# Kernel tuning notes

Hardware: AMD Instinct MI355X
Metric: run time of the kernel (lower is better)

The kernel has to match this reference:

```python
import jax, jax.numpy as jnp
import numpy as np

NUM_HEADS = 8
HIDDEN = 128
MAX_NEIGHBORS = 64
BATCH = 8192


def setup_inputs() -> dict:
    key = jax.random.key(0)
    ks = jax.random.split(key, 4)
    query = jax.random.normal(ks[0], (BATCH, MAX_NEIGHBORS, HIDDEN), dtype=jnp.float32)
    value = jax.random.normal(ks[1], (BATCH, 1, HIDDEN), dtype=jnp.float32)
    # per-head Dense(hidden) weights (glorot-ish scale) + zero biases
    Wa = jax.random.normal(ks[2], (NUM_HEADS, HIDDEN, HIDDEN), dtype=jnp.float32) * (1.0 / np.sqrt(HIDDEN))
    ba = jnp.zeros((NUM_HEADS, HIDDEN), dtype=jnp.float32)
    Wo = jax.random.normal(ks[3], (NUM_HEADS * HIDDEN, HIDDEN), dtype=jnp.float32) * (1.0 / np.sqrt(NUM_HEADS * HIDDEN))
    bo = jnp.zeros((HIDDEN,), dtype=jnp.float32)
    return {"query": query, "value": value, "Wa": Wa, "ba": ba, "Wo": Wo, "bo": bo}


def reference(query, value, Wa, ba, Wo, bo):
    # query: [B, N, H], value: [B, 1, H]
    q = jnp.concatenate([query, value], axis=1)  # [B, N+1, H]
    contexts = []
    for i in range(NUM_HEADS):
        # sequential per-head projection of the running query tensor
        q = jnp.einsum('bnh,hk->bnk', q, Wa[i]) + ba[i]          # [B, N+1, H]
        e = jnp.einsum('boh,bnh->bon', value, q)                 # [B, 1, N+1]
        scores = jax.nn.softmax(e, axis=-1)                      # [B, 1, N+1]
        contexts.append(jnp.einsum('bon,bnh->boh', scores, q))   # [B, 1, H]
    ctx = jnp.concatenate(contexts, axis=-1)                     # [B, 1, num_heads*H]
    x = jnp.einsum('boc,ck->bok', ctx, Wo) + bo                  # [B, 1, H]
    return jax.nn.relu(x)
```

## Files before the change

kernel.cpp:

```cpp
#include <hip/hip_runtime.h>
#include <math.h>

#define WS_P  0
#define WS_Q0 65536
#define WS_Q1 81920
#define WS_R  98304
#define WS_WT 114688
#define WS_WU 245760
#define WS_ZT 376832
#define WS_Z0 507904
#define WS_U  524288
#define WS_PO 8912896

struct MMJob { const float* A; const float* B; float* C; float* wu; };
struct MMArgs { MMJob j[8]; };

__device__ __forceinline__ float dpp_xor1(float x) {
  return __int_as_float(__builtin_amdgcn_update_dpp(0, __float_as_int(x), 0xB1, 0xF, 0xF, false));
}
__device__ __forceinline__ float dpp_xor2(float x) {
  return __int_as_float(__builtin_amdgcn_update_dpp(0, __float_as_int(x), 0x4E, 0xF, 0xF, false));
}
__device__ __forceinline__ float dpp_xor8(float x) {
  return __int_as_float(__builtin_amdgcn_update_dpp(0, __float_as_int(x), 0x128, 0xF, 0xF, false));
}
__device__ __forceinline__ float readlane_f(float v, int n) {
  return __int_as_float(__builtin_amdgcn_readlane(__float_as_int(v), n));
}

__device__ void mm128_job(const MMJob J, const int tile, const int t, float* Al) {
  const int col = t & 127;
  const int rg = t >> 7;
  if (J.A == nullptr) {
    for (int rr = 0; rr < 16; ++rr) {
      const int r = tile * 32 + rg * 16 + rr;
      const float v = J.B[r * 128 + col];
      if (J.C) J.C[r * 128 + col] = v;
      if (J.wu) J.wu[col * 1024 + r] = v;
    }
    return;
  }
  for (int jj = 0; jj < 16; ++jj) {
    const int idx = t + jj * 256;
    Al[idx] = J.A[tile * 32 * 128 + idx];
  }
  __syncthreads();
  float acc[16];
#pragma unroll
  for (int rr = 0; rr < 16; ++rr) acc[rr] = 0.f;
  for (int h = 0; h < 128; ++h) {
    const float bv = J.B[h * 128 + col];
#pragma unroll
    for (int rr = 0; rr < 16; ++rr)
      acc[rr] = fmaf(Al[(rg * 16 + rr) * 128 + h], bv, acc[rr]);
  }
#pragma unroll
  for (int rr = 0; rr < 16; ++rr) {
    const int r = tile * 32 + rg * 16 + rr;
    if (J.C) J.C[r * 128 + col] = acc[rr];
    if (J.wu) J.wu[col * 1024 + r] = acc[rr];
  }
}

__global__ __launch_bounds__(256) void k1_setup(MMArgs args,
    const float* __restrict__ Wa, const float* __restrict__ ba,
    const float* __restrict__ Wo, const float* __restrict__ bo,
    float* __restrict__ z0) {
  __shared__ float smem[4096];
  const int t = threadIdx.x;
  if (blockIdx.x < 16) {
    mm128_job(args.j[blockIdx.x >> 2], blockIdx.x & 3, t, smem);
    return;
  }
  float* bt = smem;
  float* zpart = smem + 1024;
  if (t < 128) bt[t] = ba[t];
  __syncthreads();
  for (int i = 1; i < 8; ++i) {
    if (t < 128) {
      float v = ba[i * 128 + t];
      for (int h = 0; h < 128; ++h)
        v = fmaf(bt[(i - 1) * 128 + h], Wa[i * 16384 + h * 128 + t], v);
      bt[i * 128 + t] = v;
    }
    __syncthreads();
  }
  const int col = t & 127, half = t >> 7;
  float z = half ? 0.f : bo[col];
  for (int i = half * 4; i < half * 4 + 4; ++i)
    for (int h = 0; h < 128; ++h)
      z = fmaf(bt[i * 128 + h], Wo[(i * 128 + h) * 128 + col], z);
  zpart[half * 128 + col] = z;
  __syncthreads();
  if (t < 128) z0[t] = zpart[t] + zpart[128 + t];
}

__global__ __launch_bounds__(256) void mm128_jobs(MMArgs args) {
  __shared__ float smem[4096];
  mm128_job(args.j[blockIdx.x >> 2], blockIdx.x & 3, threadIdx.x, smem);
}

__device__ void gemm_U_dev(const float* __restrict__ V, const float* __restrict__ WU,
                           float* __restrict__ U, const int bid, const int t, float* Vl) {
  const int rt = bid >> 3;
  const int ct = bid & 7;
  const int cg = t & 7;
  const int rg = t >> 3;
  const int r0 = rt * 128;
  float4 acc[4][4];
#pragma unroll
  for (int a = 0; a < 4; ++a)
#pragma unroll
    for (int c = 0; c < 4; ++c) acc[a][c] = make_float4(0.f, 0.f, 0.f, 0.f);
  for (int kc = 0; kc < 4; ++kc) {
    __syncthreads();
    {
      const int srow = t >> 3, k8 = t & 7;
#pragma unroll
      for (int pp = 0; pp < 4; ++pp) {
        const int rr = pp * 32 + srow;
        *(float4*)&Vl[rr * 33 + k8 * 4] =
            *(const float4*)&V[(size_t)(r0 + rr) * 128 + kc * 32 + k8 * 4];
      }
    }
    __syncthreads();
#pragma unroll 4
    for (int kk = 0; kk < 32; ++kk) {
      const float* wrow = WU + (size_t)(kc * 32 + kk) * 1024 + ct * 128 + cg * 16;
      const float4 w0 = *(const float4*)(wrow + 0);
      const float4 w1 = *(const float4*)(wrow + 4);
      const float4 w2 = *(const float4*)(wrow + 8);
      const float4 w3 = *(const float4*)(wrow + 12);
#pragma unroll
      for (int r = 0; r < 4; ++r) {
        const float s = Vl[(rg * 4 + r) * 33 + kk];
        acc[r][0].x = fmaf(s, w0.x, acc[r][0].x); acc[r][0].y = fmaf(s, w0.y, acc[r][0].y);
        acc[r][0].z = fmaf(s, w0.z, acc[r][0].z); acc[r][0].w = fmaf(s, w0.w, acc[r][0].w);
        acc[r][1].x = fmaf(s, w1.x, acc[r][1].x); acc[r][1].y = fmaf(s, w1.y, acc[r][1].y);
        acc[r][1].z = fmaf(s, w1.z, acc[r][1].z); acc[r][1].w = fmaf(s, w1.w, acc[r][1].w);
        acc[r][2].x = fmaf(s, w2.x, acc[r][2].x); acc[r][2].y = fmaf(s, w2.y, acc[r][2].y);
        acc[r][2].z = fmaf(s, w2.z, acc[r][2].z); acc[r][2].w = fmaf(s, w2.w, acc[r][2].w);
        acc[r][3].x = fmaf(s, w3.x, acc[r][3].x); acc[r][3].y = fmaf(s, w3.y, acc[r][3].y);
        acc[r][3].z = fmaf(s, w3.z, acc[r][3].z); acc[r][3].w = fmaf(s, w3.w, acc[r][3].w);
      }
    }
  }
#pragma unroll
  for (int r = 0; r < 4; ++r) {
    float* urow = U + (size_t)(r0 + rg * 4 + r) * 1024 + ct * 128 + cg * 16;
    *(float4*)(urow + 0) = acc[r][0];
    *(float4*)(urow + 4) = acc[r][1];
    *(float4*)(urow + 8) = acc[r][2];
    *(float4*)(urow + 12) = acc[r][3];
  }
}

__global__ __launch_bounds__(256) void k4_combo(MMArgs args,
    const float* __restrict__ V, const float* __restrict__ WU, float* __restrict__ U) {
  __shared__ float smem[4224];
  const int bid = blockIdx.x;
  if (bid < 32) mm128_job(args.j[bid >> 2], bid & 3, threadIdx.x, smem);
  else gemm_U_dev(V, WU, U, bid - 32, threadIdx.x, smem);
}

#define ATTN_NB 4

__global__ __launch_bounds__(256, 4) void attn_main_k(
    const float* __restrict__ query, const float* __restrict__ value,
    float* __restrict__ U) {
  __shared__ float smem[4948];
  float* sct = smem + 4420;
  const int t = threadIdx.x;
  const int w = t >> 6;
  const int l = t & 63;

  const int sel1 = l & 1, sel2 = (l >> 1) & 1, sel8 = (l >> 3) & 1;
  const int g = ((l >> 2) & 1) | (((l >> 4) & 1) << 1) | (((l >> 5) & 1) << 2);
  const int myhead = 4 * sel1 + 2 * sel2 + sel8;
  const int ebase = myhead * 8 + g;

#pragma unroll 1
  for (int j = 0; j < ATTN_NB; ++j) {
    const int b = blockIdx.x * ATTN_NB + j;

    float2 u2[8];
    {
      const float* ub = U + (size_t)b * 1024 + 2 * l;
#pragma unroll
      for (int i = 0; i < 8; ++i) u2[i] = *(const float2*)(ub + i * 128);
    }
    float2 q2[16];
    {
      const float* qb = query + (size_t)b * 8192 + (size_t)(w * 16) * 128 + 2 * l;
#pragma unroll
      for (int r = 0; r < 16; ++r) q2[r] = *(const float2*)(qb + r * 128);
    }
    const float2 v2 = *(const float2*)(value + (size_t)b * 128 + 2 * l);

    auto epass = [&](const float2 qv, const int n) {
      float p[8];
#pragma unroll
      for (int i = 0; i < 8; ++i) p[i] = fmaf(qv.y, u2[i].y, qv.x * u2[i].x);
      float a4[4];
#pragma unroll
      for (int i = 0; i < 4; ++i) {
        const float yours = sel1 ? p[i] : p[i + 4];
        const float mine = sel1 ? p[i + 4] : p[i];
        a4[i] = mine + dpp_xor1(yours);
      }
      float a2v[2];
#pragma unroll
      for (int i = 0; i < 2; ++i) {
        const float yours = sel2 ? a4[i] : a4[i + 2];
        const float mine = sel2 ? a4[i + 2] : a4[i];
        a2v[i] = mine + dpp_xor2(yours);
      }
      const float yours = sel8 ? a2v[0] : a2v[1];
      const float mine = sel8 ? a2v[1] : a2v[0];
      smem[n * 68 + ebase] = mine + dpp_xor8(yours);
    };
#pragma unroll
    for (int r = 0; r < 16; ++r) epass(q2[r], 16 * w + r);
    if (w == 0) epass(v2, 64);
    __syncthreads();

#pragma unroll
    for (int ii = 0; ii < 2; ++ii) {
      const int i = 2 * w + ii;
      const float4 e0 = *(const float4*)&smem[l * 68 + i * 8];
      const float4 e1 = *(const float4*)&smem[l * 68 + i * 8 + 4];
      const float4 f0 = *(const float4*)&smem[64 * 68 + i * 8];
      const float4 f1 = *(const float4*)&smem[64 * 68 + i * 8 + 4];
      const float x = ((e0.x + e0.y) + (e0.z + e0.w)) + ((e1.x + e1.y) + (e1.z + e1.w));
      const float x64 = ((f0.x + f0.y) + (f0.z + f0.w)) + ((f1.x + f1.y) + (f1.z + f1.w));
      float m = x;
      m = fmaxf(m, dpp_xor1(m));
      m = fmaxf(m, dpp_xor2(m));
      m = fmaxf(m, __shfl_xor(m, 4));
      m = fmaxf(m, dpp_xor8(m));
      m = fmaxf(m, __shfl_xor(m, 16));
      m = fmaxf(m, __shfl_xor(m, 32));
      m = fmaxf(m, x64);
      const float p = __expf(x - m);
      const float p64 = __expf(x64 - m);
      float ss = p;
      ss += dpp_xor1(ss);
      ss += dpp_xor2(ss);
      ss += __shfl_xor(ss, 4);
      ss += dpp_xor8(ss);
      ss += __shfl_xor(ss, 16);
      ss += __shfl_xor(ss, 32);
      ss += p64;
      const float inv = 1.0f / ss;
      sct[i * 66 + l] = p * inv;
      if (l == 0) sct[i * 66 + 64] = p64 * inv;
    }
    __syncthreads();

    float sc[8], c64[8];
#pragma unroll
    for (int i = 0; i < 8; ++i) sc[i] = sct[i * 66 + l];
#pragma unroll
    for (int i = 0; i < 8; ++i) c64[i] = sct[i * 66 + 64];

    float2 s2[8];
#pragma unroll
    for (int i = 0; i < 8; ++i) s2[i] = make_float2(0.f, 0.f);
#pragma unroll
    for (int r = 0; r < 16; ++r) {
      const int n = 16 * w + r;
#pragma unroll
      for (int i = 0; i < 8; ++i) {
        const float cwv = readlane_f(sc[i], n);
        s2[i].x = fmaf(cwv, q2[r].x, s2[i].x);
        s2[i].y = fmaf(cwv, q2[r].y, s2[i].y);
      }
    }
    if (w == 0) {
#pragma unroll
      for (int i = 0; i < 8; ++i) {
        s2[i].x = fmaf(c64[i], v2.x, s2[i].x);
        s2[i].y = fmaf(c64[i], v2.y, s2[i].y);
      }
    }
#pragma unroll
    for (int i = 0; i < 8; ++i)
      *(float2*)&smem[w * 1024 + i * 128 + 2 * l] = s2[i];
    __syncthreads();
    float4 acc = make_float4(0.f, 0.f, 0.f, 0.f);
#pragma unroll
    for (int w4 = 0; w4 < 4; ++w4) {
      const float4 pp = *(const float4*)&smem[w4 * 1024 + t * 4];
      acc.x += pp.x; acc.y += pp.y; acc.z += pp.z; acc.w += pp.w;
    }
    *(float4*)(U + (size_t)b * 1024 + t * 4) = acc;
    __syncthreads();
  }
}

__global__ __launch_bounds__(256) void gemm_out_k(
    const float* __restrict__ S, const float* __restrict__ Z,
    float* __restrict__ P0, float* __restrict__ PW) {
  __shared__ float STl[64 * 68];
  const int rb = blockIdx.x >> 2;
  const int kc = blockIdx.x & 3;
  const int t = threadIdx.x;
  const int rg = t >> 4;
  const int cg = t & 15;
  float4 acc[4][2];
#pragma unroll
  for (int r = 0; r < 4; ++r) {
    acc[r][0] = make_float4(0.f, 0.f, 0.f, 0.f);
    acc[r][1] = make_float4(0.f, 0.f, 0.f, 0.f);
  }
  for (int sub = 0; sub < 4; ++sub) {
    const int kb = kc * 256 + sub * 64;
    __syncthreads();
#pragma unroll
    for (int j = 0; j < 4; ++j) {
      const int i4 = t + j * 256;
      const int row = i4 >> 4, kq = i4 & 15;
      const float4 s4 = *(const float4*)&S[(size_t)(rb * 64 + row) * 1024 + kb + kq * 4];
      STl[(kq * 4 + 0) * 68 + row] = s4.x;
      STl[(kq * 4 + 1) * 68 + row] = s4.y;
      STl[(kq * 4 + 2) * 68 + row] = s4.z;
      STl[(kq * 4 + 3) * 68 + row] = s4.w;
    }
    __syncthreads();
#pragma unroll 4
    for (int k = 0; k < 64; ++k) {
      const float4 sa = *(const float4*)&STl[k * 68 + rg * 4];
      const float* zr = Z + (size_t)(kb + k) * 128 + cg * 8;
      const float4 za = *(const float4*)zr;
      const float4 zb = *(const float4*)(zr + 4);
      const float sr[4] = {sa.x, sa.y, sa.z, sa.w};
#pragma unroll
      for (int r = 0; r < 4; ++r) {
        acc[r][0].x = fmaf(sr[r], za.x, acc[r][0].x);
        acc[r][0].y = fmaf(sr[r], za.y, acc[r][0].y);
        acc[r][0].z = fmaf(sr[r], za.z, acc[r][0].z);
        acc[r][0].w = fmaf(sr[r], za.w, acc[r][0].w);
        acc[r][1].x = fmaf(sr[r], zb.x, acc[r][1].x);
        acc[r][1].y = fmaf(sr[r], zb.y, acc[r][1].y);
        acc[r][1].z = fmaf(sr[r], zb.z, acc[r][1].z);
        acc[r][1].w = fmaf(sr[r], zb.w, acc[r][1].w);
      }
    }
  }
  float* P = (kc == 0) ? P0 : (PW + (size_t)(kc - 1) * 1048576);
#pragma unroll
  for (int r = 0; r < 4; ++r) {
    float* prow = P + (size_t)(rb * 64 + rg * 4 + r) * 128 + cg * 8;
    *(float4*)(prow + 0) = acc[r][0];
    *(float4*)(prow + 4) = acc[r][1];
  }
}

__global__ __launch_bounds__(256) void reduce_relu_k(
    float* __restrict__ out, const float* __restrict__ PW,
    const float* __restrict__ z0) {
  const int idx = blockIdx.x * 256 + threadIdx.x;
  const float4 z4 = *(const float4*)&z0[(idx & 31) * 4];
  float4 a = ((const float4*)out)[idx];
  const float4 p1 = ((const float4*)(PW + 0 * 1048576))[idx];
  const float4 p2 = ((const float4*)(PW + 1 * 1048576))[idx];
  const float4 p3 = ((const float4*)(PW + 2 * 1048576))[idx];
  a.x = fmaxf(a.x + p1.x + p2.x + p3.x + z4.x, 0.f);
  a.y = fmaxf(a.y + p1.y + p2.y + p3.y + z4.y, 0.f);
  a.z = fmaxf(a.z + p1.z + p2.z + p3.z + z4.z, 0.f);
  a.w = fmaxf(a.w + p1.w + p2.w + p3.w + z4.w, 0.f);
  ((float4*)out)[idx] = a;
}

extern "C" void kernel_launch(void* const* d_in, const int* in_sizes, int n_in,
                              void* d_out, int out_size, void* d_ws, size_t ws_size,
                              hipStream_t stream) {
  const float* query = (const float*)d_in[0];
  const float* value = (const float*)d_in[1];
  const float* Wa    = (const float*)d_in[2];
  const float* ba    = (const float*)d_in[3];
  const float* Wo    = (const float*)d_in[4];
  const float* bo    = (const float*)d_in[5];
  float* ws = (float*)d_ws;
  float* P  = ws + WS_P;
  float* Q0 = ws + WS_Q0;
  float* Q1 = ws + WS_Q1;
  float* R  = ws + WS_R;
  float* WT = ws + WS_WT;
  float* WU = ws + WS_WU;
  float* ZT = ws + WS_ZT;
  float* Z0 = ws + WS_Z0;
  float* U  = ws + WS_U;
  float* PW = ws + WS_PO;

  MMArgs a1{};
  for (int j = 0; j < 4; ++j)
    a1.j[j] = MMJob{Wa + 2 * j * 16384, Wa + (2 * j + 1) * 16384, P + j * 16384, nullptr};
  k1_setup<<<17, 256, 0, stream>>>(a1, Wa, ba, Wo, bo, Z0);

  MMArgs a2{};
  a2.j[0] = MMJob{P, P + 16384, Q0, nullptr};
  a2.j[1] = MMJob{P + 2 * 16384, P + 3 * 16384, Q1, nullptr};
  a2.j[2] = MMJob{P + 2 * 16384, Wa + 6 * 16384, R, nullptr};
  mm128_jobs<<<12, 256, 0, stream>>>(a2);

  MMArgs a3{};
  a3.j[0] = MMJob{nullptr, Wa,             WT + 0 * 16384, WU + 0 * 128};
  a3.j[1] = MMJob{nullptr, P,              WT + 1 * 16384, WU + 1 * 128};
  a3.j[2] = MMJob{P,       Wa + 2 * 16384, WT + 2 * 16384, WU + 2 * 128};
  a3.j[3] = MMJob{nullptr, Q0,             WT + 3 * 16384, WU + 3 * 128};
  a3.j[4] = MMJob{Q0,      Wa + 4 * 16384, WT + 4 * 16384, WU + 4 * 128};
  a3.j[5] = MMJob{Q0,      P + 2 * 16384,  WT + 5 * 16384, WU + 5 * 128};
  a3.j[6] = MMJob{Q0,      R,              WT + 6 * 16384, WU + 6 * 128};
  a3.j[7] = MMJob{Q0,      Q1,             WT + 7 * 16384, WU + 7 * 128};
  mm128_jobs<<<32, 256, 0, stream>>>(a3);

  MMArgs a4{};
  for (int i = 0; i < 8; ++i)
    a4.j[i] = MMJob{WT + i * 16384, Wo + i * 16384, ZT + i * 16384, nullptr};
  k4_combo<<<544, 256, 0, stream>>>(a4, value, WU, U);

  attn_main_k<<<8192 / ATTN_NB, 256, 0, stream>>>(query, value, U);

  gemm_out_k<<<512, 256, 0, stream>>>(U, ZT, (float*)d_out, PW);
  reduce_relu_k<<<1024, 256, 0, stream>>>((float*)d_out, PW, Z0);
}
```

Before: 265.0 us.

## Launch one attention block per batch row and move bias chain into combo kernel

```diff
diff --git a/kernel.cpp b/kernel.cpp
--- a/kernel.cpp
+++ b/kernel.cpp
@@ -62,16 +62,14 @@
   }
 }
 
-__global__ __launch_bounds__(256) void k1_setup(MMArgs args,
-    const float* __restrict__ Wa, const float* __restrict__ ba,
-    const float* __restrict__ Wo, const float* __restrict__ bo,
-    float* __restrict__ z0) {
+__global__ __launch_bounds__(256) void mm128_jobs(MMArgs args) {
   __shared__ float smem[4096];
-  const int t = threadIdx.x;
-  if (blockIdx.x < 16) {
-    mm128_job(args.j[blockIdx.x >> 2], blockIdx.x & 3, t, smem);
-    return;
-  }
+  mm128_job(args.j[blockIdx.x >> 2], blockIdx.x & 3, threadIdx.x, smem);
+}
+
+__device__ void bias_z0_dev(const float* __restrict__ Wa, const float* __restrict__ ba,
+                            const float* __restrict__ Wo, const float* __restrict__ bo,
+                            float* __restrict__ z0, const int t, float* smem) {
   float* bt = smem;
   float* zpart = smem + 1024;
   if (t < 128) bt[t] = ba[t];
@@ -93,11 +91,6 @@
   zpart[half * 128 + col] = z;
   __syncthreads();
   if (t < 128) z0[t] = zpart[t] + zpart[128 + t];
-}
-
-__global__ __launch_bounds__(256) void mm128_jobs(MMArgs args) {
-  __shared__ float smem[4096];
-  mm128_job(args.j[blockIdx.x >> 2], blockIdx.x & 3, threadIdx.x, smem);
 }
 
 __device__ void gemm_U_dev(const float* __restrict__ V, const float* __restrict__ WU,
@@ -156,20 +149,23 @@
 }
 
 __global__ __launch_bounds__(256) void k4_combo(MMArgs args,
-    const float* __restrict__ V, const float* __restrict__ WU, float* __restrict__ U) {
+    const float* __restrict__ V, const float* __restrict__ WU, float* __restrict__ U,
+    const float* __restrict__ Wa, const float* __restrict__ ba,
+    const float* __restrict__ Wo, const float* __restrict__ bo,
+    float* __restrict__ z0) {
   __shared__ float smem[4224];
   const int bid = blockIdx.x;
   if (bid < 32) mm128_job(args.j[bid >> 2], bid & 3, threadIdx.x, smem);
-  else gemm_U_dev(V, WU, U, bid - 32, threadIdx.x, smem);
-}
-
-#define ATTN_NB 4
+  else if (bid < 544) gemm_U_dev(V, WU, U, bid - 32, threadIdx.x, smem);
+  else bias_z0_dev(Wa, ba, Wo, bo, z0, threadIdx.x, smem);
+}
 
 __global__ __launch_bounds__(256, 4) void attn_main_k(
     const float* __restrict__ query, const float* __restrict__ value,
     float* __restrict__ U) {
   __shared__ float smem[4948];
   float* sct = smem + 4420;
+  const int b = blockIdx.x;
   const int t = threadIdx.x;
   const int w = t >> 6;
   const int l = t & 63;
@@ -179,123 +175,107 @@
   const int myhead = 4 * sel1 + 2 * sel2 + sel8;
   const int ebase = myhead * 8 + g;
 
-#pragma unroll 1
-  for (int j = 0; j < ATTN_NB; ++j) {
-    const int b = blockIdx.x * ATTN_NB + j;
-
-    float2 u2[8];
-    {
-      const float* ub = U + (size_t)b * 1024 + 2 * l;
-#pragma unroll
-      for (int i = 0; i < 8; ++i) u2[i] = *(const float2*)(ub + i * 128);
-    }
-    float2 q2[16];
-    {
-      const float* qb = query + (size_t)b * 8192 + (size_t)(w * 16) * 128 + 2 * l;
-#pragma unroll
-      for (int r = 0; r < 16; ++r) q2[r] = *(const float2*)(qb + r * 128);
-    }
-    const float2 v2 = *(const float2*)(value + (size_t)b * 128 + 2 * l);
-
-    auto epass = [&](const float2 qv, const int n) {
-      float p[8];
-#pragma unroll
-      for (int i = 0; i < 8; ++i) p[i] = fmaf(qv.y, u2[i].y, qv.x * u2[i].x);
-      float a4[4];
-#pragma unroll
-      for (int i = 0; i < 4; ++i) {
-        const float yours = sel1 ? p[i] : p[i + 4];
-        const float mine = sel1 ? p[i + 4] : p[i];
-        a4[i] = mine + dpp_xor1(yours);
-      }
-      float a2v[2];
-#pragma unroll
-      for (int i = 0; i < 2; ++i) {
-        const float yours = sel2 ? a4[i] : a4[i + 2];
-        const float mine = sel2 ? a4[i + 2] : a4[i];
-        a2v[i] = mine + dpp_xor2(yours);
-      }
-      const float yours = sel8 ? a2v[0] : a2v[1];
-      const float mine = sel8 ? a2v[1] : a2v[0];
-      smem[n * 68 + ebase] = mine + dpp_xor8(yours);
-    };
-#pragma unroll
-    for (int r = 0; r < 16; ++r) epass(q2[r], 16 * w + r);
-    if (w == 0) epass(v2, 64);
-    __syncthreads();
-
-#pragma unroll
-    for (int ii = 0; ii < 2; ++ii) {
-      const int i = 2 * w + ii;
-      const float4 e0 = *(const float4*)&smem[l * 68 + i * 8];
-      const float4 e1 = *(const float4*)&smem[l * 68 + i * 8 + 4];
-      const float4 f0 = *(const float4*)&smem[64 * 68 + i * 8];
-      const float4 f1 = *(const float4*)&smem[64 * 68 + i * 8 + 4];
-      const float x = ((e0.x + e0.y) + (e0.z + e0.w)) + ((e1.x + e1.y) + (e1.z + e1.w));
-      const float x64 = ((f0.x + f0.y) + (f0.z + f0.w)) + ((f1.x + f1.y) + (f1.z + f1.w));
-      float m = x;
-      m = fmaxf(m, dpp_xor1(m));
-      m = fmaxf(m, dpp_xor2(m));
-      m = fmaxf(m, __shfl_xor(m, 4));
-      m = fmaxf(m, dpp_xor8(m));
-      m = fmaxf(m, __shfl_xor(m, 16));
-      m = fmaxf(m, __shfl_xor(m, 32));
-      m = fmaxf(m, x64);
-      const float p = __expf(x - m);
-      const float p64 = __expf(x64 - m);
-      float ss = p;
-      ss += dpp_xor1(ss);
-      ss += dpp_xor2(ss);
-      ss += __shfl_xor(ss, 4);
-      ss += dpp_xor8(ss);
-      ss += __shfl_xor(ss, 16);
-      ss += __shfl_xor(ss, 32);
-      ss += p64;
-      const float inv = 1.0f / ss;
-      sct[i * 66 + l] = p * inv;
-      if (l == 0) sct[i * 66 + 64] = p64 * inv;
-    }
-    __syncthreads();
-
-    float sc[8], c64[8];
-#pragma unroll
-    for (int i = 0; i < 8; ++i) sc[i] = sct[i * 66 + l];
-#pragma unroll
-    for (int i = 0; i < 8; ++i) c64[i] = sct[i * 66 + 64];
-
-    float2 s2[8];
-#pragma unroll
-    for (int i = 0; i < 8; ++i) s2[i] = make_float2(0.f, 0.f);
-#pragma unroll
-    for (int r = 0; r < 16; ++r) {
-      const int n = 16 * w + r;
-#pragma unroll
-      for (int i = 0; i < 8; ++i) {
-        const float cwv = readlane_f(sc[i], n);
-        s2[i].x = fmaf(cwv, q2[r].x, s2[i].x);
-        s2[i].y = fmaf(cwv, q2[r].y, s2[i].y);
-      }
-    }
-    if (w == 0) {
-#pragma unroll
-      for (int i = 0; i < 8; ++i) {
-        s2[i].x = fmaf(c64[i], v2.x, s2[i].x);
-        s2[i].y = fmaf(c64[i], v2.y, s2[i].y);
-      }
-    }
-#pragma unroll
-    for (int i = 0; i < 8; ++i)
-      *(float2*)&smem[w * 1024 + i * 128 + 2 * l] = s2[i];
-    __syncthreads();
-    float4 acc = make_float4(0.f, 0.f, 0.f, 0.f);
-#pragma unroll
-    for (int w4 = 0; w4 < 4; ++w4) {
-      const float4 pp = *(const float4*)&smem[w4 * 1024 + t * 4];
-      acc.x += pp.x; acc.y += pp.y; acc.z += pp.z; acc.w += pp.w;
-    }
-    *(float4*)(U + (size_t)b * 1024 + t * 4) = acc;
-    __syncthreads();
-  }
+  float2 u2[8];
+  {
+    const float* ub = U + (size_t)b * 1024 + 2 * l;
+#pragma unroll
+    for (int jj = 0; jj < 8; ++jj) u2[jj] = *(const float2*)(ub + ((myhead ^ jj) << 7));
+  }
+  float2 q2[16];
+  {
+    const float* qb = query + (size_t)b * 8192 + (size_t)(w * 16) * 128 + 2 * l;
+#pragma unroll
+    for (int r = 0; r < 16; ++r) q2[r] = *(const float2*)(qb + r * 128);
+  }
+  const float2 v2 = *(const float2*)(value + (size_t)b * 128 + 2 * l);
+
+  auto epass = [&](const float2 qv, const int n) {
+    float p[8];
+#pragma unroll
+    for (int i = 0; i < 8; ++i) p[i] = fmaf(qv.y, u2[i].y, qv.x * u2[i].x);
+    float a4[4];
+#pragma unroll
+    for (int i = 0; i < 4; ++i) a4[i] = p[i] + dpp_xor1(p[i + 4]);
+    float a2v[2];
+#pragma unroll
+    for (int i = 0; i < 2; ++i) a2v[i] = a4[i] + dpp_xor2(a4[i + 2]);
+    smem[n * 68 + ebase] = a2v[0] + dpp_xor8(a2v[1]);
+  };
+#pragma unroll
+  for (int r = 0; r < 16; ++r) epass(q2[r], 16 * w + r);
+  if (w == 0) epass(v2, 64);
+  __syncthreads();
+
+#pragma unroll
+  for (int ii = 0; ii < 2; ++ii) {
+    const int i = 2 * w + ii;
+    const float4 e0 = *(const float4*)&smem[l * 68 + i * 8];
+    const float4 e1 = *(const float4*)&smem[l * 68 + i * 8 + 4];
+    const float4 f0 = *(const float4*)&smem[64 * 68 + i * 8];
+    const float4 f1 = *(const float4*)&smem[64 * 68 + i * 8 + 4];
+    const float x = ((e0.x + e0.y) + (e0.z + e0.w)) + ((e1.x + e1.y) + (e1.z + e1.w));
+    const float x64 = ((f0.x + f0.y) + (f0.z + f0.w)) + ((f1.x + f1.y) + (f1.z + f1.w));
+    float m = x;
+    m = fmaxf(m, dpp_xor1(m));
+    m = fmaxf(m, dpp_xor2(m));
+    m = fmaxf(m, __shfl_xor(m, 4));
+    m = fmaxf(m, dpp_xor8(m));
+    m = fmaxf(m, __shfl_xor(m, 16));
+    m = fmaxf(m, __shfl_xor(m, 32));
+    m = fmaxf(m, x64);
+    const float p = __expf(x - m);
+    const float p64 = __expf(x64 - m);
+    float ss = p;
+    ss += dpp_xor1(ss);
+    ss += dpp_xor2(ss);
+    ss += __shfl_xor(ss, 4);
+    ss += dpp_xor8(ss);
+    ss += __shfl_xor(ss, 16);
+    ss += __shfl_xor(ss, 32);
+    ss += p64;
+    const float inv = 1.0f / ss;
+    sct[i * 66 + l] = p * inv;
+    if (l == 0) sct[i * 66 + 64] = p64 * inv;
+  }
+  __syncthreads();
+
+  float sc[8], c64[8];
+#pragma unroll
+  for (int i = 0; i < 8; ++i) sc[i] = sct[i * 66 + l];
+#pragma unroll
+  for (int i = 0; i < 8; ++i) c64[i] = sct[i * 66 + 64];
+
+  float2 s2[8];
+#pragma unroll
+  for (int i = 0; i < 8; ++i) s2[i] = make_float2(0.f, 0.f);
+#pragma unroll
+  for (int r = 0; r < 16; ++r) {
+    const int n = 16 * w + r;
+#pragma unroll
+    for (int i = 0; i < 8; ++i) {
+      const float cwv = readlane_f(sc[i], n);
+      s2[i].x = fmaf(cwv, q2[r].x, s2[i].x);
+      s2[i].y = fmaf(cwv, q2[r].y, s2[i].y);
+    }
+  }
+  if (w == 0) {
+#pragma unroll
+    for (int i = 0; i < 8; ++i) {
+      s2[i].x = fmaf(c64[i], v2.x, s2[i].x);
+      s2[i].y = fmaf(c64[i], v2.y, s2[i].y);
+    }
+  }
+#pragma unroll
+  for (int i = 0; i < 8; ++i)
+    *(float2*)&smem[w * 1024 + i * 128 + 2 * l] = s2[i];
+  __syncthreads();
+  float4 acc = make_float4(0.f, 0.f, 0.f, 0.f);
+#pragma unroll
+  for (int w4 = 0; w4 < 4; ++w4) {
+    const float4 pp = *(const float4*)&smem[w4 * 1024 + t * 4];
+    acc.x += pp.x; acc.y += pp.y; acc.z += pp.z; acc.w += pp.w;
+  }
+  *(float4*)(U + (size_t)b * 1024 + t * 4) = acc;
 }
 
 __global__ __launch_bounds__(256) void gemm_out_k(
@@ -396,7 +376,7 @@
   MMArgs a1{};
   for (int j = 0; j < 4; ++j)
     a1.j[j] = MMJob{Wa + 2 * j * 16384, Wa + (2 * j + 1) * 16384, P + j * 16384, nullptr};
-  k1_setup<<<17, 256, 0, stream>>>(a1, Wa, ba, Wo, bo, Z0);
+  mm128_jobs<<<16, 256, 0, stream>>>(a1);
 
   MMArgs a2{};
   a2.j[0] = MMJob{P, P + 16384, Q0, nullptr};
@@ -418,9 +398,9 @@
   MMArgs a4{};
   for (int i = 0; i < 8; ++i)
     a4.j[i] = MMJob{WT + i * 16384, Wo + i * 16384, ZT + i * 16384, nullptr};
-  k4_combo<<<544, 256, 0, stream>>>(a4, value, WU, U);
-
-  attn_main_k<<<8192 / ATTN_NB, 256, 0, stream>>>(query, value, U);
+  k4_combo<<<545, 256, 0, stream>>>(a4, value, WU, U, Wa, ba, Wo, bo, Z0);
+
+  attn_main_k<<<8192, 256, 0, stream>>>(query, value, U);
 
   gemm_out_k<<<512, 256, 0, stream>>>(U, ZT, (float*)d_out, PW);
   reduce_relu_k<<<1024, 256, 0, stream>>>((float*)d_out, PW, Z0);
```

After: 220.7 us, median of 3. -16.7%, faster.
